# Optimization experiments

Measured on AMD Instinct MI355X. Metric: run time of the kernel, lower is better.

## Reference

```python
import jax, jax.numpy as jnp
import numpy as np

B, T, I, H, L = 128, 256, 512, 1024, 2


def setup_inputs() -> dict:
    key = jax.random.key(0)
    ks = jax.random.split(key, 9)
    s_i = 1.0 / np.sqrt(H)
    inp = {
        "x": jax.random.normal(ks[0], (B, T, I), dtype=jnp.float32),
        # layer 0: input_size -> hidden_size
        "W_ih0": jax.random.uniform(ks[1], (4 * H, I), dtype=jnp.float32, minval=-s_i, maxval=s_i),
        "W_hh0": jax.random.uniform(ks[2], (4 * H, H), dtype=jnp.float32, minval=-s_i, maxval=s_i),
        "b_ih0": jax.random.uniform(ks[3], (4 * H,), dtype=jnp.float32, minval=-s_i, maxval=s_i),
        "b_hh0": jax.random.uniform(ks[4], (4 * H,), dtype=jnp.float32, minval=-s_i, maxval=s_i),
        # layer 1: hidden_size -> hidden_size
        "W_ih1": jax.random.uniform(ks[5], (4 * H, H), dtype=jnp.float32, minval=-s_i, maxval=s_i),
        "W_hh1": jax.random.uniform(ks[6], (4 * H, H), dtype=jnp.float32, minval=-s_i, maxval=s_i),
        "b_ih1": jax.random.uniform(ks[7], (4 * H,), dtype=jnp.float32, minval=-s_i, maxval=s_i),
        "b_hh1": jax.random.uniform(ks[8], (4 * H,), dtype=jnp.float32, minval=-s_i, maxval=s_i),
    }
    return inp


def _lstm_cell(xt, h, c, W_ih, W_hh, b_ih, b_hh):
    # gates: [B, 4H] in order i, f, g, o (standard LSTMCell layout)
    gates = xt @ W_ih.T + b_ih + h @ W_hh.T + b_hh
    i, f, g, o = jnp.split(gates, 4, axis=-1)
    c_new = jax.nn.sigmoid(f) * c + jax.nn.sigmoid(i) * jnp.tanh(g)
    h_new = jax.nn.sigmoid(o) * jnp.tanh(c_new)
    return h_new, c_new


def reference(x, W_ih0, W_hh0, b_ih0, b_hh0, W_ih1, W_hh1, b_ih1, b_hh1):
    batch = x.shape[0]
    hidden = W_hh0.shape[1]
    params = ((W_ih0, W_hh0, b_ih0, b_hh0), (W_ih1, W_hh1, b_ih1, b_hh1))
    z = jnp.zeros((batch, hidden), dtype=x.dtype)
    # torch code initializes h and c both from h0 (zeros)
    init = (tuple(z for _ in params), tuple(z for _ in params))

    def step(carry, xt):
        hs, cs = carry
        new_h, new_c = [], []
        layer_in = xt
        for l, (Wi, Wh, bi, bh) in enumerate(params):
            h2, c2 = _lstm_cell(layer_in, hs[l], cs[l], Wi, Wh, bi, bh)
            new_h.append(h2)
            new_c.append(c2)
            layer_in = h2
        return (tuple(new_h), tuple(new_c)), layer_in

    xs = jnp.swapaxes(x, 0, 1)  # [T, B, I]
    _, ys = jax.lax.scan(step, init, xs)
    out = jnp.swapaxes(ys, 0, 1)  # [B, T, H]
    return out
```

## Files before the change

kernel.cpp:

```cpp
#include <hip/hip_runtime.h>

#define B_ 128
#define T_ 256
#define I_ 512
#define H_ 1024

typedef _Float16 f16;
typedef _Float16 v8h __attribute__((ext_vector_type(8)));
typedef _Float16 v2h __attribute__((ext_vector_type(2)));
typedef float v16f __attribute__((ext_vector_type(16)));
typedef int v4i __attribute__((ext_vector_type(4)));

__device__ __forceinline__ float fsigmoid(float x) { return 1.0f / (1.0f + __expf(-x)); }
__device__ __forceinline__ float ftanh(float x) { return 1.0f - 2.0f / (__expf(2.0f * x) + 1.0f); }

__device__ __forceinline__ void gl_lds16(const void* g, void* l) {
    __builtin_amdgcn_global_load_lds(
        (const __attribute__((address_space(1))) unsigned int*)g,
        (__attribute__((address_space(3))) unsigned int*)l, 16, 0, 0);
}
__device__ __forceinline__ void gl_lds16_coh(const void* g, void* l) {
    __builtin_amdgcn_global_load_lds(
        (const __attribute__((address_space(1))) unsigned int*)g,
        (__attribute__((address_space(3))) unsigned int*)l, 16, 0, 17);
}

__device__ __forceinline__ void pollwait2(const int* baseA, int tA,
                                          const int* baseB, int tB, int lane) {
    if (tA <= 0 && tB <= 0) return;
    for (;;) {
        bool ok = true;
        if (lane < 32) {
            const int* b = (lane < 16) ? baseA : baseB;
            const int t = (lane < 16) ? tA : tB;
            v4i v;
            asm volatile("global_load_dwordx4 %0, %1, off sc0 sc1\n\ts_waitcnt vmcnt(0)"
                         : "=&v"(v) : "v"(b + (lane & 15) * 4) : "memory");
            ok = (t <= 0) || ((v[0] >= t) && (v[1] >= t) && (v[2] >= t) && (v[3] >= t));
        }
        if (__ballot(ok) == ~0ULL) return;
        __builtin_amdgcn_s_sleep(4);
    }
}

#define WAITV(n) asm volatile("s_waitcnt vmcnt(" #n ")" ::: "memory")
#define BARX { __builtin_amdgcn_s_barrier(); __builtin_amdgcn_sched_barrier(0); }

__global__ void k_f32_to_f16(const float* __restrict__ in, f16* __restrict__ out, int n) {
    int i = blockIdx.x * blockDim.x + threadIdx.x;
    int st = gridDim.x * blockDim.x;
    for (; i < n; i += st) out[i] = (f16)in[i];
}
__global__ void k_bias_sum(const float* __restrict__ a, const float* __restrict__ b,
                           float* __restrict__ o, int n) {
    int i = blockIdx.x * blockDim.x + threadIdx.x;
    int st = gridDim.x * blockDim.x;
    for (; i < n; i += st) o[i] = a[i] + b[i];
}

template <int SLOT>
__device__ void run_slot9(int mh, int tile,
                          const f16* __restrict__ xh,
                          const f16* __restrict__ wi, const f16* __restrict__ wh,
                          const float* __restrict__ bs,
                          f16* __restrict__ h0, f16* __restrict__ h1,
                          float* __restrict__ out, int* flags, char* lds)
{
    constexpr int K0 = SLOT ? 1024 : 512;
    constexpr int KW = SLOT ? 512 : 384;
    constexpr int NR = KW / 64;
    constexpr int NKS = KW / 16;
    const size_t BH = (size_t)B_ * H_;

    const int tid = threadIdx.x;
    const int wave = tid >> 6;
    const int lane = tid & 63;
    const int l31 = lane & 31, khi = lane >> 5;
    const int nw = wave & 1, kw = wave >> 1;
    const int n0 = tile * 16;
    const int rbase = mh * 64;

    const int gcl = nw * 32 + l31;
    const size_t gr = (size_t)(gcl >> 4) * H_ + n0 + (gcl & 15);
    v8h wfrag[NKS];
#pragma unroll
    for (int s = 0; s < NKS; ++s) {
        const int k = kw * KW + s * 16 + khi * 8;
        const f16* p = (k < K0) ? (wi + gr * K0 + k) : (wh + gr * H_ + (k - K0));
        wfrag[s] = *(const v8h*)p;
    }

    const int urow = tid >> 3;
    const int un = (tid & 7) * 2;
    const float2 bI = *(const float2*)(bs + 0 * H_ + n0 + un);
    const float2 bF = *(const float2*)(bs + 1 * H_ + n0 + un);
    const float2 bG = *(const float2*)(bs + 2 * H_ + n0 + un);
    const float2 bO = *(const float2*)(bs + 3 * H_ + n0 + un);
    float c0r = 0.f, c1r = 0.f;

    int* f_pub = flags + (SLOT * 2 + mh) * 64;
    const int* fA = flags + mh * 64;
    const int* fB = flags + (2 + mh) * 64;

    float* gf = (float*)(lds + 49152);

    const int rw_ = lane >> 3;
    const int ss_ = (lane & 7) ^ rw_;

#pragma unroll 1
    for (int p = 0; p <= T_; ++p) {
        const bool active = SLOT ? (p >= 1) : (p < T_);
        const int tau = SLOT ? p - 1 : p;

        const f16* srcA = nullptr; size_t strA = 0; const f16* srcB = nullptr; f16* hout = nullptr;
        if (active) {
            if (SLOT == 0) {
                srcA = xh + (size_t)tau * I_;  strA = (size_t)T_ * I_;
                srcB = h0 + (size_t)((p + 3) & 3) * BH;
                hout = h0 + (size_t)(p & 3) * BH;
            } else {
                srcA = h0 + (size_t)((p + 3) & 3) * BH;  strA = H_;
                srcB = h1 + (size_t)((p + 3) & 3) * BH;
                hout = h1 + (size_t)(p & 3) * BH;
            }
        }

        auto issue = [&](int r) {
            const int kc = kw * KW + r * 64;
            const f16* base; size_t str; int koff; bool coh;
            if (kc < K0) { base = srcA; str = strA; koff = kc; coh = (SLOT == 1); }
            else         { base = srcB; str = (size_t)H_; koff = kc - K0; coh = true; }
            char* dbase = lds + kw * 40960 + (r % 5) * 8192 + nw * 4096;
#pragma unroll
            for (int i = 0; i < 4; ++i) {
                const int rl = rbase + nw * 32 + i * 8 + rw_;
                const f16* gp = base + (size_t)rl * str + koff + ss_ * 8;
                if (coh) gl_lds16_coh(gp, dbase + i * 1024);
                else     gl_lds16(gp, dbase + i * 1024);
            }
        };

        v16f acc0 = {}, acc1 = {};

        auto compute = [&](int r) {
            const char* sb = lds + kw * 40960 + (r % 5) * 8192;
#pragma unroll
            for (int ks = 0; ks < 4; ++ks) {
                const int qo = (((ks * 2 + khi) ^ (l31 & 7)) << 4);
                const v8h a0 = *(const v8h*)(sb + l31 * 128 + qo);
                const v8h a1 = *(const v8h*)(sb + (32 + l31) * 128 + qo);
                __builtin_amdgcn_s_setprio(1);
                acc0 = __builtin_amdgcn_mfma_f32_32x32x16_f16(a0, wfrag[r * 4 + ks], acc0, 0, 0, 0);
                acc1 = __builtin_amdgcn_mfma_f32_32x32x16_f16(a1, wfrag[r * 4 + ks], acc1, 0, 0, 0);
                __builtin_amdgcn_s_setprio(0);
            }
        };

        if (active) {
            unsigned premask = 0;
            if (SLOT == 0) {
#pragma unroll
                for (int r = 0; r < 4; ++r)
                    if (kw * KW + r * 64 + 64 <= K0) { issue(r); premask |= 1u << r; }
            }

            if (wave == 0) pollwait2(fA, p, fB, SLOT ? p : p - 2, lane);
            __syncthreads();
            __builtin_amdgcn_sched_barrier(0);

#pragma unroll
            for (int r = 0; r < 4; ++r)
                if (!(premask & (1u << r))) issue(r);

#pragma unroll
            for (int r = 0; r < NR; ++r) {
                if (r + 4 <= NR)      WAITV(12);
                else if (r + 3 == NR) WAITV(8);
                else if (r + 2 == NR) WAITV(4);
                else                  WAITV(0);
                BARX;
                if (r + 4 < NR) issue(r + 4);
                compute(r);
            }
            __syncthreads();

            if (kw >= 1) {
                float* rg = (float*)lds + ((kw - 1) * 2 + nw) * 2048;
#pragma unroll
                for (int j = 0; j < 16; ++j) {
                    rg[j * 64 + lane] = acc0[j];
                    rg[(16 + j) * 64 + lane] = acc1[j];
                }
            }
            __syncthreads();
            if (kw == 0) {
                const float* r0 = (float*)lds + (0 + nw) * 2048;
                const float* r1 = (float*)lds + (2 + nw) * 2048;
                const float* r2 = (float*)lds + (4 + nw) * 2048;
#pragma unroll
                for (int j = 0; j < 16; ++j) {
                    const float s0 = acc0[j] + r0[j * 64 + lane] + r1[j * 64 + lane] + r2[j * 64 + lane];
                    const float s1 = acc1[j] + r0[(16 + j) * 64 + lane] + r1[(16 + j) * 64 + lane] + r2[(16 + j) * 64 + lane];
                    const int row = (j & 3) + 8 * (j >> 2) + 4 * khi;
                    gf[row * 68 + nw * 32 + l31] = s0;
                    gf[(32 + row) * 68 + nw * 32 + l31] = s1;
                }
            }
            __syncthreads();

            {
                const float* g0 = gf + urow * 68 + un;
                const float xi0 = g0[0] + bI.x,  xi1 = g0[1] + bI.y;
                const float xf0 = g0[16] + bF.x, xf1 = g0[17] + bF.y;
                const float xg0 = g0[32] + bG.x, xg1 = g0[33] + bG.y;
                const float xo0 = g0[48] + bO.x, xo1 = g0[49] + bO.y;
                const float cn0 = fsigmoid(xf0) * c0r + fsigmoid(xi0) * ftanh(xg0);
                const float cn1 = fsigmoid(xf1) * c1r + fsigmoid(xi1) * ftanh(xg1);
                const float hn0 = fsigmoid(xo0) * ftanh(cn0);
                const float hn1 = fsigmoid(xo1) * ftanh(cn1);
                c0r = cn0; c1r = cn1;
                union { v2h h2; unsigned u; } cv;
                cv.h2[0] = (f16)hn0; cv.h2[1] = (f16)hn1;
                unsigned* hp = (unsigned*)(hout + (size_t)(rbase + urow) * H_ + n0 + un);
                asm volatile("global_store_dword %0, %1, off sc0 sc1" :: "v"(hp), "v"(cv.u) : "memory");
                if (SLOT == 1) {
                    float2 yv; yv.x = hn0; yv.y = hn1;
                    *(float2*)(out + ((size_t)(rbase + urow) * T_ + tau) * H_ + n0 + un) = yv;
                }
            }
        }

        asm volatile("s_waitcnt vmcnt(0)" ::: "memory");
        __syncthreads();
        if (tid == 0) {
            int v = p + 1;
            int* fp = f_pub + tile;
            asm volatile("global_store_dword %0, %1, off sc0 sc1" :: "v"(fp), "v"(v) : "memory");
        }
    }
}

__global__ __launch_bounds__(512, 2) void lstm_persist9(
    const f16* __restrict__ xh,
    const f16* __restrict__ w0i, const f16* __restrict__ w0h,
    const f16* __restrict__ w1i, const f16* __restrict__ w1h,
    const float* __restrict__ bs0, const float* __restrict__ bs1,
    f16* __restrict__ h0, f16* __restrict__ h1, float* __restrict__ out,
    int* flags)
{
    __shared__ __align__(16) char lds[163840];
    const int bx = blockIdx.x;
    const int slot = bx & 1;
    const int mh = (bx >> 1) & 1;
    const int tile = bx >> 2;
    if (slot == 0)
        run_slot9<0>(mh, tile, xh, w0i, w0h, bs0, h0, h1, out, flags, lds);
    else
        run_slot9<1>(mh, tile, xh, w1i, w1h, bs1, h0, h1, out, flags, lds);
}

#define BM 64
#define NT 8

__global__ __launch_bounds__(256) void lstm_step(
    const float* __restrict__ A1, long a1_stride, int K1,
    const float* __restrict__ hprev,
    const float* __restrict__ Wih, const float* __restrict__ Whh,
    const float* __restrict__ bih, const float* __restrict__ bhh,
    float* __restrict__ cbuf, float* __restrict__ hout,
    float* yout, long y_stride)
{
    __shared__ float As[32][66];
    __shared__ float Ws[32][36];
    const int tid = threadIdx.x;
    const int n0 = blockIdx.x * NT;
    const int b0 = blockIdx.y * BM;
    const int tb = tid >> 3;
    const int tc = tid & 7;
    const int lr = tid >> 3;
    const int lk = tid & 7;
    const long wj = (long)(lr >> 3) * H_ + n0 + (lr & 7);
    float acc[2][4] = {{0.f, 0.f, 0.f, 0.f}, {0.f, 0.f, 0.f, 0.f}};
#pragma unroll 1
    for (int ph = 0; ph < 2; ++ph) {
        const float* Ap = (ph == 0) ? A1 : hprev;
        const long as = (ph == 0) ? a1_stride : (long)H_;
        const float* W = (ph == 0) ? Wih : Whh;
        const int K = (ph == 0) ? K1 : H_;
        const float* arow0 = Ap + (long)(b0 + lr) * as + 4 * lk;
        const float* arow1 = Ap + (long)(b0 + lr + 32) * as + 4 * lk;
        const float* wrow = W + wj * K + 4 * lk;
        float4 ra0 = *(const float4*)(arow0);
        float4 ra1 = *(const float4*)(arow1);
        float4 rw = *(const float4*)(wrow);
        for (int k0 = 0; k0 < K; k0 += 32) {
            __syncthreads();
            {
                const int kk = 4 * lk;
                As[kk + 0][lr] = ra0.x; As[kk + 1][lr] = ra0.y;
                As[kk + 2][lr] = ra0.z; As[kk + 3][lr] = ra0.w;
                As[kk + 0][lr + 32] = ra1.x; As[kk + 1][lr + 32] = ra1.y;
                As[kk + 2][lr + 32] = ra1.z; As[kk + 3][lr + 32] = ra1.w;
                Ws[kk + 0][lr] = rw.x; Ws[kk + 1][lr] = rw.y;
                Ws[kk + 2][lr] = rw.z; Ws[kk + 3][lr] = rw.w;
            }
            __syncthreads();
            const int kn = k0 + 32;
            if (kn < K) {
                ra0 = *(const float4*)(arow0 + kn);
                ra1 = *(const float4*)(arow1 + kn);
                rw = *(const float4*)(wrow + kn);
            }
#pragma unroll
            for (int k = 0; k < 32; ++k) {
                float2 a = *(const float2*)&As[k][2 * tb];
                float4 w = *(const float4*)&Ws[k][4 * tc];
                acc[0][0] = fmaf(a.x, w.x, acc[0][0]);
                acc[0][1] = fmaf(a.x, w.y, acc[0][1]);
                acc[0][2] = fmaf(a.x, w.z, acc[0][2]);
                acc[0][3] = fmaf(a.x, w.w, acc[0][3]);
                acc[1][0] = fmaf(a.y, w.x, acc[1][0]);
                acc[1][1] = fmaf(a.y, w.y, acc[1][1]);
                acc[1][2] = fmaf(a.y, w.z, acc[1][2]);
                acc[1][3] = fmaf(a.y, w.w, acc[1][3]);
            }
        }
    }
    __syncthreads();
    float* gsf = &As[0][0];
#pragma unroll
    for (int bi = 0; bi < 2; ++bi)
#pragma unroll
        for (int ci = 0; ci < 4; ++ci)
            gsf[(2 * tb + bi) * 33 + 4 * tc + ci] = acc[bi][ci];
    __syncthreads();
    const int dn = tid & 7;
    const int bq = tid >> 3;
    const int n = n0 + dn;
#pragma unroll
    for (int s = 0; s < 2; ++s) {
        const int b = bq + 32 * s;
        float xi = gsf[b * 33 + dn] + bih[n] + bhh[n];
        float xf = gsf[b * 33 + 8 + dn] + bih[H_ + n] + bhh[H_ + n];
        float xg = gsf[b * 33 + 16 + dn] + bih[2 * H_ + n] + bhh[2 * H_ + n];
        float xo = gsf[b * 33 + 24 + dn] + bih[3 * H_ + n] + bhh[3 * H_ + n];
        const long idx = (long)(b0 + b) * H_ + n;
        const float c_old = cbuf[idx];
        const float cn = fsigmoid(xf) * c_old + fsigmoid(xi) * ftanh(xg);
        const float hn = fsigmoid(xo) * ftanh(cn);
        cbuf[idx] = cn;
        hout[idx] = hn;
        if (yout) yout[(long)(b0 + b) * y_stride + n] = hn;
    }
}

extern "C" void kernel_launch(void* const* d_in, const int* in_sizes, int n_in,
                              void* d_out, int out_size, void* d_ws, size_t ws_size,
                              hipStream_t stream) {
    const float* x = (const float*)d_in[0];
    const float* Wih0 = (const float*)d_in[1];
    const float* Whh0 = (const float*)d_in[2];
    const float* bih0 = (const float*)d_in[3];
    const float* bhh0 = (const float*)d_in[4];
    const float* Wih1 = (const float*)d_in[5];
    const float* Whh1 = (const float*)d_in[6];
    const float* bih1 = (const float*)d_in[7];
    const float* bhh1 = (const float*)d_in[8];
    float* out = (float*)d_out;

    const size_t BH = (size_t)B_ * H_;
    const size_t NX = (size_t)B_ * T_ * I_;
    const size_t NW0I = (size_t)4 * H_ * I_;
    const size_t NWH = (size_t)4 * H_ * H_;

    const size_t off_xh = 0;
    const size_t off_w0i = off_xh + NX * 2;
    const size_t off_w0h = off_w0i + NW0I * 2;
    const size_t off_w1i = off_w0h + NWH * 2;
    const size_t off_w1h = off_w1i + NWH * 2;
    const size_t off_bs0 = off_w1h + NWH * 2;
    const size_t off_bs1 = off_bs0 + 4 * H_ * 4;
    const size_t off_h0 = off_bs1 + 4 * H_ * 4;
    const size_t off_h1 = off_h0 + 4 * BH * 2;
    const size_t off_flags = off_h1 + 4 * BH * 2;
    const size_t REQ = off_flags + 256 * 4;

    char* ws = (char*)d_ws;

    if (ws_size >= REQ) {
        f16* xh = (f16*)(ws + off_xh);
        f16* w0i = (f16*)(ws + off_w0i);
        f16* w0h = (f16*)(ws + off_w0h);
        f16* w1i = (f16*)(ws + off_w1i);
        f16* w1h = (f16*)(ws + off_w1h);
        float* bs0 = (float*)(ws + off_bs0);
        float* bs1 = (float*)(ws + off_bs1);
        f16* h0 = (f16*)(ws + off_h0);
        f16* h1 = (f16*)(ws + off_h1);
        int* flags = (int*)(ws + off_flags);

        hipMemsetAsync(ws + off_h0, 0, REQ - off_h0, stream);

        dim3 cb(256);
        k_f32_to_f16<<<2048, cb, 0, stream>>>(x, xh, (int)NX);
        k_f32_to_f16<<<2048, cb, 0, stream>>>(Wih0, w0i, (int)NW0I);
        k_f32_to_f16<<<2048, cb, 0, stream>>>(Whh0, w0h, (int)NWH);
        k_f32_to_f16<<<2048, cb, 0, stream>>>(Wih1, w1i, (int)NWH);
        k_f32_to_f16<<<2048, cb, 0, stream>>>(Whh1, w1h, (int)NWH);
        k_bias_sum<<<16, cb, 0, stream>>>(bih0, bhh0, bs0, 4 * H_);
        k_bias_sum<<<16, cb, 0, stream>>>(bih1, bhh1, bs1, 4 * H_);

        lstm_persist9<<<256, 512, 0, stream>>>(xh, w0i, w0h, w1i, w1h, bs0, bs1,
                                               h0, h1, out, flags);
        return;
    }

    float* fws = (float*)d_ws;
    float* h0a = fws;
    float* h0b = fws + BH;
    float* c0 = fws + 2 * BH;
    float* h1a = fws + 3 * BH;
    float* h1b = fws + 4 * BH;
    float* c1 = fws + 5 * BH;
    hipMemsetAsync(d_ws, 0, 6 * BH * sizeof(float), stream);

    dim3 grid(H_ / NT, B_ / BM);
    dim3 block(256);
    for (int t = 0; t < T_; ++t) {
        float* h0in = (t & 1) ? h0b : h0a;
        float* h0out = (t & 1) ? h0a : h0b;
        float* h1in = (t & 1) ? h1b : h1a;
        float* h1out = (t & 1) ? h1a : h1b;
        lstm_step<<<grid, block, 0, stream>>>(
            x + (size_t)t * I_, (long)T_ * I_, I_,
            h0in, Wih0, Whh0, bih0, bhh0, c0, h0out, nullptr, 0);
        lstm_step<<<grid, block, 0, stream>>>(
            h0out, (long)H_, H_,
            h1in, Wih1, Whh1, bih1, bhh1, c1, h1out,
            out + (size_t)t * H_, (long)T_ * H_);
    }
}
```

Measured before the change: 2.239 ms.

## Rebalance layer-0 K split, publish flag before output store, shorten poll sleep

Layer 0 now gives every k-wave an equal slice of the input part (128) and the recurrent part (256), instead of splitting the concatenated K contiguously. Each wave can therefore prefetch its two input chunks before waiting on the dependency flags, which should shorten the critical path. The step-done flag is now published before the layer-1 fp32 output store, so that store no longer delays dependent blocks. The poll sleep is also halved, trading more polling traffic for lower wake-up latency.

```diff
diff --git a/kernel.cpp b/kernel.cpp
--- a/kernel.cpp
+++ b/kernel.cpp
@@ -39,7 +39,7 @@
             ok = (t <= 0) || ((v[0] >= t) && (v[1] >= t) && (v[2] >= t) && (v[3] >= t));
         }
         if (__ballot(ok) == ~0ULL) return;
-        __builtin_amdgcn_s_sleep(4);
+        __builtin_amdgcn_s_sleep(2);
     }
 }
 
@@ -59,17 +59,15 @@
 }
 
 template <int SLOT>
-__device__ void run_slot9(int mh, int tile,
+__device__ void run_slotA(int mh, int tile,
                           const f16* __restrict__ xh,
                           const f16* __restrict__ wi, const f16* __restrict__ wh,
                           const float* __restrict__ bs,
                           f16* __restrict__ h0, f16* __restrict__ h1,
                           float* __restrict__ out, int* flags, char* lds)
 {
-    constexpr int K0 = SLOT ? 1024 : 512;
-    constexpr int KW = SLOT ? 512 : 384;
-    constexpr int NR = KW / 64;
-    constexpr int NKS = KW / 16;
+    constexpr int NR = SLOT ? 8 : 6;
+    constexpr int NKS = NR * 4;
     const size_t BH = (size_t)B_ * H_;
 
     const int tid = threadIdx.x;
@@ -85,8 +83,14 @@
     v8h wfrag[NKS];
 #pragma unroll
     for (int s = 0; s < NKS; ++s) {
-        const int k = kw * KW + s * 16 + khi * 8;
-        const f16* p = (k < K0) ? (wi + gr * K0 + k) : (wh + gr * H_ + (k - K0));
+        const f16* p;
+        if (SLOT == 0) {
+            p = (s < 8) ? (wi + gr * 512 + kw * 128 + s * 16 + khi * 8)
+                        : (wh + gr * 1024 + kw * 256 + (s - 8) * 16 + khi * 8);
+        } else {
+            const int k = kw * 512 + s * 16 + khi * 8;
+            p = (k < 1024) ? (wi + gr * 1024 + k) : (wh + gr * 1024 + (k - 1024));
+        }
         wfrag[s] = *(const v8h*)p;
     }
 
@@ -119,17 +123,22 @@
                 srcB = h0 + (size_t)((p + 3) & 3) * BH;
                 hout = h0 + (size_t)(p & 3) * BH;
             } else {
-                srcA = h0 + (size_t)((p + 3) & 3) * BH;  strA = H_;
+                srcA = h0 + (size_t)((p + 3) & 3) * BH;
                 srcB = h1 + (size_t)((p + 3) & 3) * BH;
                 hout = h1 + (size_t)(p & 3) * BH;
             }
         }
 
         auto issue = [&](int r) {
-            const int kc = kw * KW + r * 64;
             const f16* base; size_t str; int koff; bool coh;
-            if (kc < K0) { base = srcA; str = strA; koff = kc; coh = (SLOT == 1); }
-            else         { base = srcB; str = (size_t)H_; koff = kc - K0; coh = true; }
+            if (SLOT == 0) {
+                if (r < 2) { base = srcA; str = strA;       koff = kw * 128 + r * 64;       coh = false; }
+                else       { base = srcB; str = (size_t)H_; koff = kw * 256 + (r - 2) * 64; coh = true; }
+            } else {
+                const int kc = kw * 512 + r * 64;
+                if (kc < 1024) { base = srcA; str = (size_t)H_; koff = kc;        coh = true; }
+                else           { base = srcB; str = (size_t)H_; koff = kc - 1024; coh = true; }
+            }
             char* dbase = lds + kw * 40960 + (r % 5) * 8192 + nw * 4096;
 #pragma unroll
             for (int i = 0; i < 4; ++i) {
@@ -157,20 +166,14 @@
         };
 
         if (active) {
-            unsigned premask = 0;
-            if (SLOT == 0) {
-#pragma unroll
-                for (int r = 0; r < 4; ++r)
-                    if (kw * KW + r * 64 + 64 <= K0) { issue(r); premask |= 1u << r; }
-            }
+            if (SLOT == 0) { issue(0); issue(1); }
 
             if (wave == 0) pollwait2(fA, p, fB, SLOT ? p : p - 2, lane);
             __syncthreads();
             __builtin_amdgcn_sched_barrier(0);
 
-#pragma unroll
-            for (int r = 0; r < 4; ++r)
-                if (!(premask & (1u << r))) issue(r);
+            if (SLOT == 0) { issue(2); issue(3); }
+            else           { issue(0); issue(1); issue(2); issue(3); }
 
 #pragma unroll
             for (int r = 0; r < NR; ++r) {
@@ -208,6 +211,7 @@
             }
             __syncthreads();
 
+            float hn0, hn1;
             {
                 const float* g0 = gf + urow * 68 + un;
                 const float xi0 = g0[0] + bI.x,  xi1 = g0[1] + bI.y;
@@ -216,31 +220,37 @@
                 const float xo0 = g0[48] + bO.x, xo1 = g0[49] + bO.y;
                 const float cn0 = fsigmoid(xf0) * c0r + fsigmoid(xi0) * ftanh(xg0);
                 const float cn1 = fsigmoid(xf1) * c1r + fsigmoid(xi1) * ftanh(xg1);
-                const float hn0 = fsigmoid(xo0) * ftanh(cn0);
-                const float hn1 = fsigmoid(xo1) * ftanh(cn1);
+                hn0 = fsigmoid(xo0) * ftanh(cn0);
+                hn1 = fsigmoid(xo1) * ftanh(cn1);
                 c0r = cn0; c1r = cn1;
                 union { v2h h2; unsigned u; } cv;
                 cv.h2[0] = (f16)hn0; cv.h2[1] = (f16)hn1;
                 unsigned* hp = (unsigned*)(hout + (size_t)(rbase + urow) * H_ + n0 + un);
                 asm volatile("global_store_dword %0, %1, off sc0 sc1" :: "v"(hp), "v"(cv.u) : "memory");
-                if (SLOT == 1) {
-                    float2 yv; yv.x = hn0; yv.y = hn1;
-                    *(float2*)(out + ((size_t)(rbase + urow) * T_ + tau) * H_ + n0 + un) = yv;
-                }
+            }
+            asm volatile("s_waitcnt vmcnt(0)" ::: "memory");
+            __syncthreads();
+            if (tid == 0) {
+                int v = p + 1;
+                int* fp = f_pub + tile;
+                asm volatile("global_store_dword %0, %1, off sc0 sc1" :: "v"(fp), "v"(v) : "memory");
+            }
+            if (SLOT == 1) {
+                float2 yv; yv.x = hn0; yv.y = hn1;
+                *(float2*)(out + ((size_t)(rbase + urow) * T_ + tau) * H_ + n0 + un) = yv;
+            }
+        } else {
+            __syncthreads();
+            if (tid == 0) {
+                int v = p + 1;
+                int* fp = f_pub + tile;
+                asm volatile("global_store_dword %0, %1, off sc0 sc1" :: "v"(fp), "v"(v) : "memory");
             }
         }
-
-        asm volatile("s_waitcnt vmcnt(0)" ::: "memory");
-        __syncthreads();
-        if (tid == 0) {
-            int v = p + 1;
-            int* fp = f_pub + tile;
-            asm volatile("global_store_dword %0, %1, off sc0 sc1" :: "v"(fp), "v"(v) : "memory");
-        }
-    }
-}
-
-__global__ __launch_bounds__(512, 2) void lstm_persist9(
+    }
+}
+
+__global__ __launch_bounds__(512, 2) void lstm_persistA(
     const f16* __restrict__ xh,
     const f16* __restrict__ w0i, const f16* __restrict__ w0h,
     const f16* __restrict__ w1i, const f16* __restrict__ w1h,
@@ -254,9 +264,9 @@
     const int mh = (bx >> 1) & 1;
     const int tile = bx >> 2;
     if (slot == 0)
-        run_slot9<0>(mh, tile, xh, w0i, w0h, bs0, h0, h1, out, flags, lds);
+        run_slotA<0>(mh, tile, xh, w0i, w0h, bs0, h0, h1, out, flags, lds);
     else
-        run_slot9<1>(mh, tile, xh, w1i, w1h, bs1, h0, h1, out, flags, lds);
+        run_slotA<1>(mh, tile, xh, w1i, w1h, bs1, h0, h1, out, flags, lds);
 }
 
 #define BM 64
@@ -410,7 +420,7 @@
         k_bias_sum<<<16, cb, 0, stream>>>(bih0, bhh0, bs0, 4 * H_);
         k_bias_sum<<<16, cb, 0, stream>>>(bih1, bhh1, bs1, 4 * H_);
 
-        lstm_persist9<<<256, 512, 0, stream>>>(xh, w0i, w0h, w1i, w1h, bs0, bs1,
+        lstm_persistA<<<256, 512, 0, stream>>>(xh, w0i, w0h, w1i, w1h, bs0, bs1,
                                                h0, h1, out, flags);
         return;
     }
```

Measured after the change: 2.250 ms. Within noise of the previous version (+0.5%).
